# Performance work log

Hardware: AMD Instinct MI355X
Metric: run time of the kernel (lower is better)

Reference implementation:

```python
import jax, jax.numpy as jnp
import numpy as np

L, B, S, D, H, F = 6, 4, 2048, 1024, 8, 2048
E = D // 8  # per-head dim, hardcoded as n_model//8 in the torch code
SCALE = E ** 0.5


def setup_inputs() -> dict:
    key = jax.random.key(0)
    ks = jax.random.split(key, 8)
    w = lambda k, shape: jax.random.normal(k, shape, jnp.float32) * 0.02
    return {
        "x": jax.random.normal(ks[0], (B, S, D), jnp.float32),
        "mask": jnp.ones((B, S), bool),
        "Wq": w(ks[1], (L, D, H * E)),
        "Wk": w(ks[2], (L, D, H * E)),
        "Wv": w(ks[3], (L, D, H * E)),
        "Wo": w(ks[4], (L, H * E, D)),
        "ln1_g": jnp.ones((L, D)), "ln1_b": jnp.zeros((L, D)),
        "W1": w(ks[5], (L, D, F)), "b1": jnp.zeros((L, F)),
        "W2": w(ks[6], (L, F, D)), "b2": jnp.zeros((L, D)),
        "ln2_g": jnp.ones((L, D)), "ln2_b": jnp.zeros((L, D)),
    }


def _ln(x, g, b):
    mu = x.mean(-1, keepdims=True)
    var = ((x - mu) ** 2).mean(-1, keepdims=True)
    return (x - mu) * jax.lax.rsqrt(var + 1e-5) * g + b


def _sin_pos(seq_len, n_model, dtype):
    # pos[t, i] = t / 10000**((i//2 * 2)/n_model); sin on even i, cos on odd i
    t = jnp.arange(seq_len, dtype=dtype)[:, None]
    i = jnp.arange(n_model)
    ang = t / (10000.0 ** (((i // 2) * 2).astype(dtype) / n_model))
    return jnp.where(i % 2 == 0, jnp.sin(ang), jnp.cos(ang))


def reference(x, mask, Wq, Wk, Wv, Wo, ln1_g, ln1_b, W1, b1, W2, b2, ln2_g, ln2_b):
    b_, s_, d_ = x.shape
    x = x + _sin_pos(s_, d_, x.dtype)  # dropout disabled (eval)
    # key-side padding mask -> additive bias [B, 1, 1, S]
    bias = jnp.where(mask, 0.0, -jnp.inf)[:, None, None, :]
    n_layers = Wq.shape[0]
    for l in range(n_layers):
        # --- multi-head attention (post-norm) ---
        q = (x @ Wq[l]).reshape(b_, s_, H, E)
        k = (x @ Wk[l]).reshape(b_, s_, H, E)
        v = (x @ Wv[l]).reshape(b_, s_, H, E)
        attn = jnp.einsum("bqhe,bkhe->bhqk", q, k) / SCALE
        attn = jax.nn.softmax(attn + bias, axis=-1)
        o = jnp.einsum("bhqk,bkhe->bqhe", attn, v).reshape(b_, s_, H * E)
        x = _ln(x + o @ Wo[l], ln1_g[l], ln1_b[l])
        # --- FFN (relu) ---
        h = jax.nn.relu(x @ W1[l] + b1[l])
        x = _ln(x + h @ W2[l] + b2[l], ln2_g[l], ln2_b[l])
    return x
```

## Files before the change

kernel.cpp:

```cpp
#include <hip/hip_runtime.h>
#include <hip/hip_bf16.h>


typedef unsigned short ushort_t;
typedef __bf16 bf16x8 __attribute__((ext_vector_type(8)));
typedef float f32x4 __attribute__((ext_vector_type(4)));
typedef unsigned short ushort8 __attribute__((ext_vector_type(8)));
typedef unsigned short ushort4v __attribute__((ext_vector_type(4)));
typedef unsigned short ushort2v __attribute__((ext_vector_type(2)));

#define DEV static __device__ __forceinline__

DEV float bf2f(ushort_t u) {
    union { unsigned int i; float f; } c; c.i = ((unsigned int)u) << 16; return c.f;
}
DEV ushort_t f2bf(float f) {
    union { float f; unsigned int i; } c; c.f = f;
    unsigned int x = c.i;
    x += 0x7fffu + ((x >> 16) & 1u);
    return (ushort_t)(x >> 16);
}
DEV float ld_in(const void* p, size_t i, int isbf) {
    return isbf ? bf2f(((const ushort_t*)p)[i]) : ((const float*)p)[i];
}

typedef __attribute__((address_space(1))) void GV;
typedef __attribute__((address_space(3))) void LV;
DEV void glds16(const ushort_t* g, ushort_t* l) {
    __builtin_amdgcn_global_load_lds((GV*)g, (LV*)l, 16, 0, 0);
}

#define LL 6
#define BB 4
#define SS 2048
#define DD 1024
#define HH 8
#define EE 128
#define FF 2048
#define HE 1024
#define MM (BB*SS)
#define QSCALE 0.12751741f

__global__ void sniff_kernel(const unsigned int* __restrict__ g1, int* __restrict__ flag)
{
    if (threadIdx.x == 0) *flag = (g1[0] == 0x3F803F80u) ? 1 : 0;
}

__global__ __launch_bounds__(256) void transpose_all_kernel(
    const void* __restrict__ Wq, const void* __restrict__ Wk,
    const void* __restrict__ Wv, const void* __restrict__ Wo,
    const void* __restrict__ W1, const void* __restrict__ W2,
    ushort_t* __restrict__ WqT, ushort_t* __restrict__ WkT,
    ushort_t* __restrict__ WvT, ushort_t* __restrict__ WoT,
    ushort_t* __restrict__ W1T, ushort_t* __restrict__ W2T,
    const int* __restrict__ flag)
{
    int isbf = *flag;
    int z = blockIdx.z; int l = z / 6, ty = z % 6;
    const void* src; ushort_t* dst; int K, N;
    switch (ty) {
        case 0: src = Wq; dst = WqT; K = DD; N = HE; break;
        case 1: src = Wk; dst = WkT; K = DD; N = HE; break;
        case 2: src = Wv; dst = WvT; K = DD; N = HE; break;
        case 3: src = Wo; dst = WoT; K = HE; N = DD; break;
        case 4: src = W1; dst = W1T; K = DD; N = FF; break;
        default: src = W2; dst = W2T; K = FF; N = DD; break;
    }
    int k0 = blockIdx.x * 32, n0 = blockIdx.y * 32;
    if (k0 >= K || n0 >= N) return;
    size_t base = (size_t)l * K * N;
    dst += base;
    __shared__ ushort_t tile[32][33];
    int tx = threadIdx.x, tyy = threadIdx.y;
    for (int i = 0; i < 4; i++)
        tile[tyy + i*8][tx] = f2bf(ld_in(src, base + (size_t)(k0 + tyy + i*8) * N + n0 + tx, isbf));
    __syncthreads();
    for (int i = 0; i < 4; i++)
        dst[(size_t)(n0 + tyy + i*8) * K + k0 + tx] = tile[tx][tyy + i*8];
}

__global__ __launch_bounds__(256) void param_convert_kernel(
    const void* __restrict__ g1, const void* __restrict__ be1,
    const void* __restrict__ g2, const void* __restrict__ be2,
    const void* __restrict__ b1, const void* __restrict__ b2,
    ushort_t* __restrict__ g1b, ushort_t* __restrict__ be1b,
    ushort_t* __restrict__ g2b, ushort_t* __restrict__ be2b,
    ushort_t* __restrict__ b1b, ushort_t* __restrict__ b2b,
    const int* __restrict__ flag)
{
    int isbf = *flag;
    const void* src; ushort_t* dst; int n;
    switch (blockIdx.z) {
        case 0: src = g1;  dst = g1b;  n = LL*DD; break;
        case 1: src = be1; dst = be1b; n = LL*DD; break;
        case 2: src = g2;  dst = g2b;  n = LL*DD; break;
        case 3: src = be2; dst = be2b; n = LL*DD; break;
        case 4: src = b1;  dst = b1b;  n = LL*FF; break;
        default: src = b2; dst = b2b;  n = LL*DD; break;
    }
    int i = blockIdx.x * 256 + threadIdx.x;
    if (i < n) dst[i] = f2bf(ld_in(src, i, isbf));
}

__global__ __launch_bounds__(256) void embed_kernel(
    const void* __restrict__ x, float* __restrict__ xf, ushort_t* __restrict__ xb,
    const int* __restrict__ flag)
{
    int isbf = *flag;
    size_t i = (size_t)blockIdx.x * 256 + threadIdx.x;
    int d = (int)(i & (DD - 1));
    int s = (int)((i >> 10) & (SS - 1));
    int i2 = d & ~1;
    float fr = __expf((float)i2 * (-9.210340371976184f / (float)DD));
    float ang = (float)s * fr;
    float pe = (d & 1) ? cosf(ang) : sinf(ang);
    float v = ld_in(x, i, isbf) + pe;
    xf[i] = v;
    xb[i] = f2bf(v);
}

template <int RELU, int HASBIAS, int VSTORE>
__global__ __launch_bounds__(256) void gemm_kernel(
    const ushort_t* __restrict__ A, const ushort_t* __restrict__ Bt,
    const ushort_t* __restrict__ bias, ushort_t* __restrict__ Cb,
    int M, int N, int K, float oscale)
{
    __shared__ __align__(16) ushort_t Alds[128 * 32];
    __shared__ __align__(16) ushort_t Blds[128 * 32];
    int t = threadIdx.x;
    size_t m0 = (size_t)blockIdx.y * 128, n0 = (size_t)blockIdx.x * 128;
    int wave = t >> 6, lane = t & 63, quad = lane >> 4, l16 = lane & 15;
    int wr = (wave >> 1) * 64, wc = (wave & 1) * 64;

    f32x4 zero = {0.f, 0.f, 0.f, 0.f};
    f32x4 acc[4][4];
    for (int i = 0; i < 4; i++) for (int j = 0; j < 4; j++) acc[i][j] = zero;

    const ushort_t* Ab = A + m0 * K;
    const ushort_t* Bb = Bt + n0 * K;
    int c0 = t, c1 = 256 + t;
    int r0 = c0 >> 2, kc0 = (c0 & 3) * 8;
    int r1 = c1 >> 2, kc1 = (c1 & 3) * 8;
    ushort_t* la0 = Alds + (size_t)(wave * 64) * 8;
    ushort_t* la1 = Alds + (size_t)(256 + wave * 64) * 8;
    ushort_t* lb0 = Blds + (size_t)(wave * 64) * 8;
    ushort_t* lb1 = Blds + (size_t)(256 + wave * 64) * 8;

    for (int k0 = 0; k0 < K; k0 += 32) {
        __syncthreads();
        glds16(Ab + (size_t)r0 * K + k0 + kc0, la0);
        glds16(Ab + (size_t)r1 * K + k0 + kc1, la1);
        glds16(Bb + (size_t)r0 * K + k0 + kc0, lb0);
        glds16(Bb + (size_t)r1 * K + k0 + kc1, lb1);
        __syncthreads();
        bf16x8 af[4], bfv[4];
        for (int i = 0; i < 4; i++)
            af[i] = *(const bf16x8*)&Alds[(wr + i * 16 + l16) * 32 + quad * 8];
        for (int j = 0; j < 4; j++)
            bfv[j] = *(const bf16x8*)&Blds[(wc + j * 16 + l16) * 32 + quad * 8];
        for (int i = 0; i < 4; i++)
            for (int j = 0; j < 4; j++)
                acc[i][j] = __builtin_amdgcn_mfma_f32_16x16x32_bf16(af[i], bfv[j], acc[i][j], 0, 0, 0);
    }

    if (VSTORE) {
        for (int j = 0; j < 4; j++) {
            size_t n = n0 + wc + j * 16 + l16;
            int hh = (int)(n >> 7), e = (int)(n & 127);
            for (int i = 0; i < 4; i++) {
                size_t mb = m0 + wr + i * 16 + quad * 4;
                int bb = (int)(mb >> 11), s = (int)(mb & 2047);
                ushort4v pw;
                for (int r = 0; r < 4; r++) pw[r] = f2bf(acc[i][j][r] * oscale);
                *(ushort4v*)&Cb[(((size_t)bb * HH + hh) * EE + e) * SS + s] = pw;
            }
        }
        return;
    }

    for (int j = 0; j < 4; j++) {
        size_t n = n0 + wc + j * 16 + l16;
        float bv = 0.f;
        if (HASBIAS) bv = bf2f(bias[n]);
        for (int i = 0; i < 4; i++) {
            size_t mb = m0 + wr + i * 16 + quad * 4;
            for (int r = 0; r < 4; r++) {
                float val = acc[i][j][r] * oscale + bv;
                if (RELU) val = fmaxf(val, 0.f);
                Cb[(mb + r) * N + n] = f2bf(val);
            }
        }
    }
}

__global__ __launch_bounds__(256) void attn_kernel(
    const ushort_t* __restrict__ Q, const ushort_t* __restrict__ Kt,
    const ushort_t* __restrict__ Vt, ushort_t* __restrict__ O)
{
    __shared__ __align__(16) ushort_t Klds[2][64 * 128];
    __shared__ __align__(16) ushort_t Vlds[2][128 * 64];
    __shared__ __align__(16) ushort_t Plds[4][16 * 72];
    int t = threadIdx.x;
    int qt = blockIdx.x, h = blockIdx.y, b = blockIdx.z;
    int wave = t >> 6, lane = t & 63, quad = lane >> 4, l16 = lane & 15;
    size_t rowbase = (size_t)b * SS;
    size_t hoff = (size_t)h * EE;

    bf16x8 qf[4];
    {
        size_t qrow = rowbase + qt * 64 + wave * 16 + l16;
        const ushort_t* qp = Q + qrow * HE + hoff;
        for (int es = 0; es < 4; es++)
            qf[es] = *(const bf16x8*)(qp + es * 32 + quad * 8);
    }

    const ushort_t* gK[4];
    const ushort_t* gV[4];
    for (int i = 0; i < 4; i++) {
        int c = t + 256 * i;
        int row = c >> 4, cc = (c & 15) ^ (row & 7);
        gK[i] = Kt + (rowbase + row) * HE + hoff + cc * 8;
    }
    for (int i = 0; i < 4; i++) {
        int c = t + 256 * i;
        int e = c >> 3, cc = (c & 7) ^ (e & 7);
        gV[i] = Vt + ((size_t)(b * HH + h) * EE + e) * SS + cc * 8;
    }

    f32x4 zero = {0.f, 0.f, 0.f, 0.f};
    f32x4 o[8];
    for (int e8 = 0; e8 < 8; e8++) o[e8] = zero;
    float m_i = -1e30f, l_i = 0.f;

    for (int i = 0; i < 4; i++) glds16(gK[i], &Klds[0][(wave * 64 + 256 * i) * 8]);
    for (int i = 0; i < 4; i++) glds16(gV[i], &Vlds[0][(wave * 64 + 256 * i) * 8]);

    const int NT = SS / 64;
    for (int kt = 0; kt < NT; kt++) {
        int cur = kt & 1;
        if (kt + 1 < NT) {
            size_t ko = (size_t)(kt + 1) * 64 * HE;
            int vo = (kt + 1) * 64;
            for (int i = 0; i < 4; i++)
                glds16(gK[i] + ko, &Klds[cur ^ 1][(wave * 64 + 256 * i) * 8]);
            for (int i = 0; i < 4; i++)
                glds16(gV[i] + vo, &Vlds[cur ^ 1][(wave * 64 + 256 * i) * 8]);
            asm volatile("s_waitcnt vmcnt(8)" ::: "memory");
        } else {
            asm volatile("s_waitcnt vmcnt(0)" ::: "memory");
        }
        __builtin_amdgcn_s_barrier();
        __builtin_amdgcn_sched_barrier(0);

        const ushort_t* Kc = Klds[cur];
        const ushort_t* Vc = Vlds[cur];

        f32x4 s[4];
        for (int kk = 0; kk < 4; kk++) s[kk] = zero;
        __builtin_amdgcn_s_setprio(1);
        for (int kk = 0; kk < 4; kk++) {
            int row = kk * 16 + l16;
            for (int es = 0; es < 4; es++) {
                int ch = (es * 4 + quad) ^ (l16 & 7);
                bf16x8 kf = *(const bf16x8*)&Kc[row * 128 + ch * 8];
                s[kk] = __builtin_amdgcn_mfma_f32_16x16x32_bf16(kf, qf[es], s[kk], 0, 0, 0);
            }
        }
        __builtin_amdgcn_s_setprio(0);

        float tm = -1e30f;
        for (int kk = 0; kk < 4; kk++)
            for (int r = 0; r < 4; r++) tm = fmaxf(tm, s[kk][r]);
        tm = fmaxf(tm, __shfl_xor(tm, 16));
        tm = fmaxf(tm, __shfl_xor(tm, 32));
        if (!__all(tm - m_i <= 8.f)) {
            float mnew = fmaxf(m_i, tm);
            float alpha = exp2f(m_i - mnew);
            float arow[4];
            for (int r = 0; r < 4; r++) arow[r] = __shfl(alpha, quad * 4 + r);
            for (int e8 = 0; e8 < 8; e8++)
                for (int r = 0; r < 4; r++) o[e8][r] *= arow[r];
            l_i *= alpha;
            m_i = mnew;
        }
        float rsum = 0.f;
        for (int kk = 0; kk < 4; kk++)
            for (int r = 0; r < 4; r++) {
                float p = exp2f(s[kk][r] - m_i);
                s[kk][r] = p; rsum += p;
            }
        rsum += __shfl_xor(rsum, 16);
        rsum += __shfl_xor(rsum, 32);
        l_i += rsum;

        for (int kk = 0; kk < 4; kk++) {
            ushort4v pw;
            for (int r = 0; r < 4; r++) pw[r] = f2bf(s[kk][r]);
            *(ushort4v*)&Plds[wave][l16 * 72 + kk * 16 + quad * 4] = pw;
        }

        __builtin_amdgcn_s_setprio(1);
        for (int kp = 0; kp < 2; kp++) {
            bf16x8 pf = *(const bf16x8*)&Plds[wave][l16 * 72 + kp * 32 + quad * 8];
            for (int e8 = 0; e8 < 8; e8++) {
                int vrow = e8 * 16 + l16;
                int ch = (kp * 4 + quad) ^ (l16 & 7);
                bf16x8 vf = *(const bf16x8*)&Vc[vrow * 64 + ch * 8];
                o[e8] = __builtin_amdgcn_mfma_f32_16x16x32_bf16(pf, vf, o[e8], 0, 0, 0);
            }
        }
        __builtin_amdgcn_s_setprio(0);

        __builtin_amdgcn_s_barrier();
    }

    float linv[4];
    for (int r = 0; r < 4; r++) linv[r] = 1.f / __shfl(l_i, quad * 4 + r);
    size_t orow0 = rowbase + qt * 64 + wave * 16 + quad * 4;
    for (int e8 = 0; e8 < 8; e8++)
        for (int r = 0; r < 4; r++)
            O[(orow0 + r) * HE + hoff + e8 * 16 + l16] = f2bf(o[e8][r] * linv[r]);
}

__global__ __launch_bounds__(256) void resid_ln_kernel(
    float* __restrict__ xf, ushort_t* __restrict__ xb,
    const ushort_t* __restrict__ pr,
    const ushort_t* __restrict__ g, const ushort_t* __restrict__ be)
{
    int row = blockIdx.x, t = threadIdx.x;
    float* xr = xf + (size_t)row * DD;
    const ushort_t* prr = pr + (size_t)row * DD;
    float v[4], s = 0.f, ss = 0.f;
    for (int i = 0; i < 4; i++) {
        int d = t + i * 256;
        v[i] = xr[d] + bf2f(prr[d]);
        s += v[i]; ss += v[i] * v[i];
    }
    for (int msk = 1; msk < 64; msk <<= 1) { s += __shfl_xor(s, msk); ss += __shfl_xor(ss, msk); }
    __shared__ float rs[4], rss[4];
    int wave = t >> 6;
    if ((t & 63) == 0) { rs[wave] = s; rss[wave] = ss; }
    __syncthreads();
    s = rs[0] + rs[1] + rs[2] + rs[3];
    ss = rss[0] + rss[1] + rss[2] + rss[3];
    float mu = s * (1.f / DD);
    float var = ss * (1.f / DD) - mu * mu;
    float rstd = rsqrtf(var + 1e-5f);
    for (int i = 0; i < 4; i++) {
        int d = t + i * 256;
        float y = (v[i] - mu) * rstd * bf2f(g[d]) + bf2f(be[d]);
        xr[d] = y;
        xb[(size_t)row * DD + d] = f2bf(y);
    }
}

__global__ __launch_bounds__(256) void out_kernel(
    const float* __restrict__ xf, void* __restrict__ out, const int* __restrict__ flag)
{
    int isbf = *flag;
    size_t i = (size_t)blockIdx.x * 256 + threadIdx.x;
    float v = xf[i];
    if (isbf) ((ushort_t*)out)[i] = f2bf(v);
    else      ((float*)out)[i] = v;
}

extern "C" void kernel_launch(void* const* d_in, const int* in_sizes, int n_in,
                              void* d_out, int out_size, void* d_ws, size_t ws_size,
                              hipStream_t stream)
{
    (void)in_sizes; (void)n_in; (void)out_size; (void)ws_size;
    const void* x   = d_in[0];
    const void* Wq  = d_in[2];
    const void* Wk  = d_in[3];
    const void* Wv  = d_in[4];
    const void* Wo  = d_in[5];
    const void* g1  = d_in[6];
    const void* be1 = d_in[7];
    const void* W1  = d_in[8];
    const void* b1  = d_in[9];
    const void* W2  = d_in[10];
    const void* b2  = d_in[11];
    const void* g2  = d_in[12];
    const void* be2 = d_in[13];

    char* w = (char*)d_ws;
    ushort_t* WqT = (ushort_t*)(w + 0);
    ushort_t* WkT = (ushort_t*)(w + 12582912);
    ushort_t* WvT = (ushort_t*)(w + 25165824);
    ushort_t* WoT = (ushort_t*)(w + 37748736);
    ushort_t* W1T = (ushort_t*)(w + 50331648);
    ushort_t* W2T = (ushort_t*)(w + 75497472);
    float*    xf  = (float*)   (w + 100663296);
    ushort_t* xb  = (ushort_t*)(w + 134217728);
    ushort_t* qb  = (ushort_t*)(w + 150994944);
    ushort_t* kb  = (ushort_t*)(w + 167772160);
    ushort_t* vt  = (ushort_t*)(w + 184549376);
    ushort_t* ao  = (ushort_t*)(w + 201326592);
    ushort_t* t0  = (ushort_t*)(w + 218103808);
    ushort_t* g1b = (ushort_t*)(w + 234881024);
    ushort_t* be1b= (ushort_t*)(w + 234893312);
    ushort_t* g2b = (ushort_t*)(w + 234905600);
    ushort_t* be2b= (ushort_t*)(w + 234917888);
    ushort_t* b1b = (ushort_t*)(w + 234930176);
    ushort_t* b2b = (ushort_t*)(w + 234954752);
    int*      flg = (int*)     (w + 234967040);
    ushort_t* hb  = qb;

    sniff_kernel<<<1, 64, 0, stream>>>((const unsigned int*)g1, flg);
    transpose_all_kernel<<<dim3(64, 64, 36), dim3(32, 8), 0, stream>>>(
        Wq, Wk, Wv, Wo, W1, W2, WqT, WkT, WvT, WoT, W1T, W2T, flg);
    param_convert_kernel<<<dim3(48, 1, 6), 256, 0, stream>>>(
        g1, be1, g2, be2, b1, b2, g1b, be1b, g2b, be2b, b1b, b2b, flg);
    embed_kernel<<<(MM * DD) / 256, 256, 0, stream>>>(x, xf, xb, flg);

    for (int l = 0; l < LL; l++) {
        const size_t o1 = (size_t)l * DD * HE, oF = (size_t)l * DD * FF;
        gemm_kernel<0, 0, 0><<<dim3(8, 64), 256, 0, stream>>>(
            xb, WqT + o1, nullptr, qb, MM, HE, DD, QSCALE);
        gemm_kernel<0, 0, 0><<<dim3(8, 64), 256, 0, stream>>>(
            xb, WkT + o1, nullptr, kb, MM, HE, DD, 1.0f);
        gemm_kernel<0, 0, 1><<<dim3(8, 64), 256, 0, stream>>>(
            xb, WvT + o1, nullptr, vt, MM, HE, DD, 1.0f);
        attn_kernel<<<dim3(SS / 64, HH, BB), 256, 0, stream>>>(qb, kb, vt, ao);
        gemm_kernel<0, 0, 0><<<dim3(8, 64), 256, 0, stream>>>(
            ao, WoT + o1, nullptr, t0, MM, DD, HE, 1.0f);
        resid_ln_kernel<<<MM, 256, 0, stream>>>(xf, xb, t0, g1b + l * DD, be1b + l * DD);
        gemm_kernel<1, 1, 0><<<dim3(16, 64), 256, 0, stream>>>(
            xb, W1T + oF, b1b + l * FF, hb, MM, FF, DD, 1.0f);
        gemm_kernel<0, 1, 0><<<dim3(8, 64), 256, 0, stream>>>(
            hb, W2T + oF, b2b + l * DD, t0, MM, DD, FF, 1.0f);
        resid_ln_kernel<<<MM, 256, 0, stream>>>(xf, xb, t0, g2b + l * DD, be2b + l * DD);
    }

    out_kernel<<<(MM * DD) / 256, 256, 0, stream>>>(xf, d_out, flg);
}
```

Before: 2.872 ms.

## Double attention query tile per block with 8 waves and XCD-aware block mapping

The attention kernel now runs 8 waves per block covering 128 query rows, so each K/V tile loaded into LDS is reused by twice as many queries. The flat block index is remapped so that (head, batch) groups land on the same XCD for better L2 sharing. The residual-layernorm kernel switches to vectorized 4-wide loads and stores, and f2bf uses the HIP intrinsic. Fewer blocks (512) may reduce occupancy balance, and the larger block raises LDS and register pressure.

```diff
diff --git a/kernel.cpp b/kernel.cpp
--- a/kernel.cpp
+++ b/kernel.cpp
@@ -15,10 +15,9 @@
     union { unsigned int i; float f; } c; c.i = ((unsigned int)u) << 16; return c.f;
 }
 DEV ushort_t f2bf(float f) {
-    union { float f; unsigned int i; } c; c.f = f;
-    unsigned int x = c.i;
-    x += 0x7fffu + ((x >> 16) & 1u);
-    return (ushort_t)(x >> 16);
+    union { __hip_bfloat16 h; ushort_t u; } c;
+    c.h = __float2bfloat16(f);
+    return c.u;
 }
 DEV float ld_in(const void* p, size_t i, int isbf) {
     return isbf ? bf2f(((const ushort_t*)p)[i]) : ((const float*)p)[i];
@@ -193,36 +192,40 @@
     }
 }
 
-__global__ __launch_bounds__(256) void attn_kernel(
+__global__ __launch_bounds__(512) void attn_kernel(
     const ushort_t* __restrict__ Q, const ushort_t* __restrict__ Kt,
     const ushort_t* __restrict__ Vt, ushort_t* __restrict__ O)
 {
     __shared__ __align__(16) ushort_t Klds[2][64 * 128];
     __shared__ __align__(16) ushort_t Vlds[2][128 * 64];
-    __shared__ __align__(16) ushort_t Plds[4][16 * 72];
+    __shared__ __align__(16) ushort_t Plds[8][16 * 72];
     int t = threadIdx.x;
-    int qt = blockIdx.x, h = blockIdx.y, b = blockIdx.z;
+    int id = blockIdx.x;
+    int xc = id & 7, y = id >> 3;
+    int hb = xc * 4 + (y & 3);
+    int qt = y >> 2;
+    int h = hb & 7, b = hb >> 3;
     int wave = t >> 6, lane = t & 63, quad = lane >> 4, l16 = lane & 15;
     size_t rowbase = (size_t)b * SS;
     size_t hoff = (size_t)h * EE;
 
     bf16x8 qf[4];
     {
-        size_t qrow = rowbase + qt * 64 + wave * 16 + l16;
+        size_t qrow = rowbase + qt * 128 + wave * 16 + l16;
         const ushort_t* qp = Q + qrow * HE + hoff;
         for (int es = 0; es < 4; es++)
             qf[es] = *(const bf16x8*)(qp + es * 32 + quad * 8);
     }
 
-    const ushort_t* gK[4];
-    const ushort_t* gV[4];
-    for (int i = 0; i < 4; i++) {
-        int c = t + 256 * i;
+    const ushort_t* gK[2];
+    const ushort_t* gV[2];
+    for (int i = 0; i < 2; i++) {
+        int c = t + 512 * i;
         int row = c >> 4, cc = (c & 15) ^ (row & 7);
         gK[i] = Kt + (rowbase + row) * HE + hoff + cc * 8;
     }
-    for (int i = 0; i < 4; i++) {
-        int c = t + 256 * i;
+    for (int i = 0; i < 2; i++) {
+        int c = t + 512 * i;
         int e = c >> 3, cc = (c & 7) ^ (e & 7);
         gV[i] = Vt + ((size_t)(b * HH + h) * EE + e) * SS + cc * 8;
     }
@@ -232,8 +235,8 @@
     for (int e8 = 0; e8 < 8; e8++) o[e8] = zero;
     float m_i = -1e30f, l_i = 0.f;
 
-    for (int i = 0; i < 4; i++) glds16(gK[i], &Klds[0][(wave * 64 + 256 * i) * 8]);
-    for (int i = 0; i < 4; i++) glds16(gV[i], &Vlds[0][(wave * 64 + 256 * i) * 8]);
+    for (int i = 0; i < 2; i++) glds16(gK[i], &Klds[0][(wave * 64 + 512 * i) * 8]);
+    for (int i = 0; i < 2; i++) glds16(gV[i], &Vlds[0][(wave * 64 + 512 * i) * 8]);
 
     const int NT = SS / 64;
     for (int kt = 0; kt < NT; kt++) {
@@ -241,11 +244,11 @@
         if (kt + 1 < NT) {
             size_t ko = (size_t)(kt + 1) * 64 * HE;
             int vo = (kt + 1) * 64;
-            for (int i = 0; i < 4; i++)
-                glds16(gK[i] + ko, &Klds[cur ^ 1][(wave * 64 + 256 * i) * 8]);
-            for (int i = 0; i < 4; i++)
-                glds16(gV[i] + vo, &Vlds[cur ^ 1][(wave * 64 + 256 * i) * 8]);
-            asm volatile("s_waitcnt vmcnt(8)" ::: "memory");
+            for (int i = 0; i < 2; i++)
+                glds16(gK[i] + ko, &Klds[cur ^ 1][(wave * 64 + 512 * i) * 8]);
+            for (int i = 0; i < 2; i++)
+                glds16(gV[i] + vo, &Vlds[cur ^ 1][(wave * 64 + 512 * i) * 8]);
+            asm volatile("s_waitcnt vmcnt(4)" ::: "memory");
         } else {
             asm volatile("s_waitcnt vmcnt(0)" ::: "memory");
         }
@@ -316,7 +319,7 @@
 
     float linv[4];
     for (int r = 0; r < 4; r++) linv[r] = 1.f / __shfl(l_i, quad * 4 + r);
-    size_t orow0 = rowbase + qt * 64 + wave * 16 + quad * 4;
+    size_t orow0 = rowbase + qt * 128 + wave * 16 + quad * 4;
     for (int e8 = 0; e8 < 8; e8++)
         for (int r = 0; r < 4; r++)
             O[(orow0 + r) * HE + hoff + e8 * 16 + l16] = f2bf(o[e8][r] * linv[r]);
@@ -330,10 +333,11 @@
     int row = blockIdx.x, t = threadIdx.x;
     float* xr = xf + (size_t)row * DD;
     const ushort_t* prr = pr + (size_t)row * DD;
+    f32x4 xv = *(const f32x4*)&xr[t * 4];
+    ushort4v pv = *(const ushort4v*)&prr[t * 4];
     float v[4], s = 0.f, ss = 0.f;
     for (int i = 0; i < 4; i++) {
-        int d = t + i * 256;
-        v[i] = xr[d] + bf2f(prr[d]);
+        v[i] = xv[i] + bf2f(pv[i]);
         s += v[i]; ss += v[i] * v[i];
     }
     for (int msk = 1; msk < 64; msk <<= 1) { s += __shfl_xor(s, msk); ss += __shfl_xor(ss, msk); }
@@ -346,12 +350,15 @@
     float mu = s * (1.f / DD);
     float var = ss * (1.f / DD) - mu * mu;
     float rstd = rsqrtf(var + 1e-5f);
+    ushort4v gv = *(const ushort4v*)&g[t * 4];
+    ushort4v bv = *(const ushort4v*)&be[t * 4];
+    f32x4 yo; ushort4v yb;
     for (int i = 0; i < 4; i++) {
-        int d = t + i * 256;
-        float y = (v[i] - mu) * rstd * bf2f(g[d]) + bf2f(be[d]);
-        xr[d] = y;
-        xb[(size_t)row * DD + d] = f2bf(y);
-    }
+        float yv = (v[i] - mu) * rstd * bf2f(gv[i]) + bf2f(bv[i]);
+        yo[i] = yv; yb[i] = f2bf(yv);
+    }
+    *(f32x4*)&xr[t * 4] = yo;
+    *(ushort4v*)&xb[(size_t)row * DD + t * 4] = yb;
 }
 
 __global__ __launch_bounds__(256) void out_kernel(
@@ -421,7 +428,7 @@
             xb, WkT + o1, nullptr, kb, MM, HE, DD, 1.0f);
         gemm_kernel<0, 0, 1><<<dim3(8, 64), 256, 0, stream>>>(
             xb, WvT + o1, nullptr, vt, MM, HE, DD, 1.0f);
-        attn_kernel<<<dim3(SS / 64, HH, BB), 256, 0, stream>>>(qb, kb, vt, ao);
+        attn_kernel<<<dim3(512), dim3(512), 0, stream>>>(qb, kb, vt, ao);
         gemm_kernel<0, 0, 0><<<dim3(8, 64), 256, 0, stream>>>(
             ao, WoT + o1, nullptr, t0, MM, DD, HE, 1.0f);
         resid_ln_kernel<<<MM, 256, 0, stream>>>(xf, xb, t0, g1b + l * DD, be1b + l * DD);
```

New measurement: 2.836 ms. Within noise of the previous version (-1.2%).
